# Performance work log

Measured on AMD Instinct MI355X. Metric: run time of the kernel, lower is better.

The kernel has to match this reference:

```python
import jax, jax.numpy as jnp
import numpy as np

H = 40  # HIDDEN_SIZE


def _gru_layer(x_tbi, Wih, Whh, bih, bhh):
    """PyTorch-convention GRU layer. x_tbi: (T, B, I). Returns (ys (T,B,H), h_T (B,H)).
    Gate order in stacked weights is (r, z, n) as in torch.nn.GRU:
      r = sigmoid(W_ir x + b_ir + W_hr h + b_hr)
      z = sigmoid(W_iz x + b_iz + W_hz h + b_hz)
      n = tanh(W_in x + b_in + r * (W_hn h + b_hn))
      h' = (1 - z) * n + z * h
    """
    # Precompute all input projections in one big GEMM: (T,B,3H)
    xg = jnp.einsum('tbi,gi->tbg', x_tbi, Wih) + bih
    B = x_tbi.shape[1]
    h0 = jnp.zeros((B, H), x_tbi.dtype)

    def step(h, xg_t):
        hg = h @ Whh.T + bhh                       # (B, 3H)
        xr, xz, xn = jnp.split(xg_t, 3, axis=-1)
        hr, hz, hn = jnp.split(hg, 3, axis=-1)
        r = jax.nn.sigmoid(xr + hr)
        z = jax.nn.sigmoid(xz + hz)
        n = jnp.tanh(xn + r * hn)
        h_new = (1.0 - z) * n + z * h
        return h_new, h_new

    hT, ys = jax.lax.scan(step, h0, xg)
    return ys, hT


def setup_inputs() -> dict:
    key = jax.random.key(0)
    ks = jax.random.split(key, 9)
    B, T, I = 4096, 256, 16
    s = 1.0 / np.sqrt(H)  # torch GRU init: U(-1/sqrt(H), 1/sqrt(H))
    u = lambda k, shape: jax.random.uniform(k, shape, jnp.float32, -s, s)
    return {
        "x": jax.random.normal(ks[0], (B, T, I), jnp.float32),
        "Wih0": u(ks[1], (3 * H, I)),
        "Whh0": u(ks[2], (3 * H, H)),
        "bih0": u(ks[3], (3 * H,)),
        "bhh0": u(ks[4], (3 * H,)),
        "Wih1": u(ks[5], (3 * H, H)),
        "Whh1": u(ks[6], (3 * H, H)),
        "bih1": u(ks[7], (3 * H,)),
        "bhh1": u(ks[8], (3 * H,)),
    }


def reference(x, Wih0, Whh0, bih0, bhh0, Wih1, Whh1, bih1, bhh1):
    # batch_first input (B,T,I) -> time-major (T,B,I) for scan
    x_tbi = jnp.transpose(x, (1, 0, 2))
    y0, _ = _gru_layer(x_tbi, Wih0, Whh0, bih0, bhh0)   # layer 0 full sequence
    _, hT = _gru_layer(y0, Wih1, Whh1, bih1, bhh1)      # layer 1 final state
    return hT  # (B, H) == h[-1]
```

## Files before the change

kernel.cpp:

```cpp
#include <hip/hip_runtime.h>

#define T_STEPS 256
#define HID 40
#define EPB 16
#define NTHR 1024
#define RR 56
#define PP (16 * RR)
#define OL1 (2 * PP)
#define STOT (4 * PP)

typedef __attribute__((ext_vector_type(8))) short bf16x8;
typedef __attribute__((ext_vector_type(4))) float f32x4;
typedef __attribute__((ext_vector_type(8))) float f32x8;
typedef __attribute__((ext_vector_type(4))) unsigned int u32x4;

__device__ __forceinline__ unsigned short bf16_rne(float v) {
    unsigned int x = __float_as_uint(v);
    unsigned int r = x + 0x7FFFu + ((x >> 16) & 1u);
    return (unsigned short)(r >> 16);
}
__device__ __forceinline__ unsigned short bf16_cvt(float v) {
    unsigned int r;
    asm("v_cvt_pk_bf16_f32 %0, %1, %2" : "=v"(r) : "v"(v), "v"(v));
    return (unsigned short)r;
}
__device__ __forceinline__ float sigm(float v) {
    return __builtin_amdgcn_rcpf(1.0f + __builtin_amdgcn_exp2f(-1.4426950408889634f * v));
}
__device__ __forceinline__ float tanh_f(float v) {
    return 1.0f - 2.0f * __builtin_amdgcn_rcpf(__builtin_amdgcn_exp2f(2.8853900817779268f * v) + 1.0f);
}

#define MF(A_, B_, C_) C_ = __builtin_amdgcn_mfma_f32_16x16x32_bf16(A_, B_, C_, 0, 0, 0)
#define PINV(v) asm volatile("" : "+v"(v))

#define BAR() do { \
    __builtin_amdgcn_sched_barrier(0); \
    asm volatile("s_waitcnt lgkmcnt(0)\n\ts_barrier" ::: "memory"); \
    __builtin_amdgcn_sched_barrier(0); \
} while (0)

__device__ bf16x8 afrag(const float* Whh, const float* Wih, int KX,
                        int rh, int rx, int c, int qrow) {
    bf16x8 f;
    #pragma unroll
    for (int j = 0; j < 8; ++j) f[j] = 0;
    #pragma unroll
    for (int j = 0; j < 8; ++j) {
        const int k = 32 * c + qrow * 8 + j;
        if (k < 40) {
            if (rh >= 0) f[j] = (short)bf16_rne(Whh[rh * 40 + k]);
        } else if (k < 40 + KX) {
            if (rx >= 0) f[j] = (short)bf16_rne(Wih[rx * KX + (k - 40)]);
        }
    }
    return f;
}

__global__ __launch_bounds__(NTHR, 4)
void gru2_kernel(const float* __restrict__ x,
                 const float* __restrict__ Wih0, const float* __restrict__ Whh0,
                 const float* __restrict__ bih0, const float* __restrict__ bhh0,
                 const float* __restrict__ Wih1, const float* __restrict__ Whh1,
                 const float* __restrict__ bih1, const float* __restrict__ bhh1,
                 float* __restrict__ out)
{
    __shared__ __align__(16) unsigned short S[STOT];

    const int tid  = threadIdx.x;
    const int wid  = tid >> 6;
    const int l    = tid & 63;
    const int col  = l & 15;
    const int qrow = l >> 4;
    const int ps   = (l & 15) & 3;
    const int pu   = (l & 15) >> 2;
    const int e0   = blockIdx.x * EPB;

    const bool isL1 = wid >= 6;
    const int  NT   = (!isL1 && wid < 4) ? 2 : 1;
    const int  TA   = isL1 ? (wid - 6) : (wid < 4 ? 2 * wid : wid + 4);
    const int  TB   = (NT == 2) ? TA + 1 : TA;
    const bool dB   = (NT != 2);

    const float* Whh = isL1 ? Whh1 : Whh0;
    const float* Wih = isL1 ? Wih1 : Wih0;
    const float* bih = isL1 ? bih1 : bih0;
    const float* bhh = isL1 ? bhh1 : bhh0;
    const int KX = isL1 ? 40 : 16;

    bf16x8 ZF;
    #pragma unroll
    for (int j = 0; j < 8; ++j) ZF[j] = 0;
    bf16x8 F00=ZF,F01=ZF,F02=ZF, F10=ZF,F11=ZF;
    f32x4 BB0, BB1;
    {
#define RRX(u, RH, RX) \
        const int RH = (ps == 2) ? -1 : (ps == 0 ? (u) : ps == 1 ? 40 + (u) : 80 + (u)); \
        const int RX = (ps == 3) ? -1 : (ps == 0 ? (u) : ps == 1 ? 40 + (u) : 80 + (u));
        {
            const int u0 = 4 * TA + pu;
            RRX(u0, rh0, rx0);
            F00 = afrag(Whh, Wih, KX, rh0, rx0, 0, qrow);
            F01 = afrag(Whh, Wih, KX, rh0, rx0, 1, qrow);
            if (isL1) F02 = afrag(Whh, Wih, KX, rh0, rx0, 2, qrow);
        }
        if (NT == 2) {
            const int u1 = 4 * TB + pu;
            RRX(u1, rh1, rx1);
            F10 = afrag(Whh, Wih, KX, rh1, rx1, 0, qrow);
            F11 = afrag(Whh, Wih, KX, rh1, rx1, 1, qrow);
        }
        const int uc0 = 4 * TA + qrow;
        const int uc1 = 4 * TB + qrow;
        BB0[0] = bih[uc0] + bhh[uc0];
        BB0[1] = bih[40 + uc0] + bhh[40 + uc0];
        BB0[2] = bih[80 + uc0];
        BB0[3] = bhh[80 + uc0];
        BB1[0] = dB ? 0.f : (bih[uc1] + bhh[uc1]);
        BB1[1] = dB ? 0.f : (bih[40 + uc1] + bhh[40 + uc1]);
        BB1[2] = dB ? 0.f : bih[80 + uc1];
        BB1[3] = dB ? 0.f : bhh[80 + uc1];
    }
    PINV(F00); PINV(F01); PINV(F02);
    PINV(F10); PINV(F11);
    PINV(BB0); PINV(BB1);

    const int rd0 = col * RR + 8 * qrow;
    const int rd1 = col * RR + 32;
    int g0, g1, g2;
    {
        auto ga = [&](int g) -> int {
            if (g < 5)  return OL1 + col * RR + 8 * g;
            if (g < 10) return col * RR + 8 * (g - 5);
            return col * RR;
        };
        g0 = ga(qrow);
        g1 = ga(4 + qrow);
        g2 = ga(8 + qrow);
    }
    const int w0  = col * RR + 4 * TA + qrow;
    const int w0b = col * RR + 4 * TB + qrow;
    const int w1  = OL1 + col * RR + 4 * TA + qrow;
    const bool usex = (qrow == 1) || (qrow == 2);
    unsigned short* Sb = &S[0];
    float hA0 = 0.f, hA1 = 0.f;

    for (int idx = tid; idx < STOT; idx += NTHR) Sb[idx] = 0;

    const float* xrow = x + (size_t)(e0 + col) * (T_STEPS * 16) + ((qrow == 2) ? 8 : 0);
    f32x8 XA, XB, XC, XD;
    #pragma unroll
    for (int j = 0; j < 8; ++j) { XA[j] = 0.f; XB[j] = 0.f; XC[j] = 0.f; XD[j] = 0.f; }
    if (!isL1) {
        XA = *(const f32x8*)(xrow);
        XB = *(const f32x8*)(xrow + 16);
        XC = *(const f32x8*)(xrow + 32);
        XD = *(const f32x8*)(xrow + 48);
    }
    __syncthreads();

#define GMATH(C, H) \
    const float r_ = sigm(C[0]); \
    const float z_ = sigm(C[1]); \
    const float n_ = tanh_f(C[2] + r_ * C[3]); \
    H = n_ + z_ * (H - n_);

#define BODY(RP, XQ) { \
    if (!isL1) { \
        if (t < T_STEPS) { \
            const bf16x8 S0 = *(const bf16x8*)(Sb + rd0 + (RP) * PP); \
            bf16x8 S1 = *(const bf16x8*)(Sb + rd1 + (RP) * PP); \
            unsigned int xw0, xw1, xw2, xw3; \
            asm("v_cvt_pk_bf16_f32 %0, %1, %2" : "=v"(xw0) : "v"(XQ[0]), "v"(XQ[1])); \
            asm("v_cvt_pk_bf16_f32 %0, %1, %2" : "=v"(xw1) : "v"(XQ[2]), "v"(XQ[3])); \
            asm("v_cvt_pk_bf16_f32 %0, %1, %2" : "=v"(xw2) : "v"(XQ[4]), "v"(XQ[5])); \
            asm("v_cvt_pk_bf16_f32 %0, %1, %2" : "=v"(xw3) : "v"(XQ[6]), "v"(XQ[7])); \
            if (t + 4 < T_STEPS) XQ = *(const f32x8*)(xrow + (t + 4) * 16); \
            u32x4 s1u = *(const u32x4*)&S1; \
            s1u[0] = usex ? xw0 : s1u[0]; \
            s1u[1] = usex ? xw1 : s1u[1]; \
            s1u[2] = usex ? xw2 : s1u[2]; \
            s1u[3] = usex ? xw3 : s1u[3]; \
            S1 = *(const bf16x8*)&s1u; \
            f32x4 c0 = __builtin_amdgcn_mfma_f32_16x16x32_bf16(F00, S0, BB0, 0, 0, 0); \
            MF(F01, S1, c0); \
            { GMATH(c0, hA0); Sb[w0 + (1 - (RP)) * PP] = bf16_cvt(hA0); } \
            if (NT == 2) { \
                f32x4 c1 = __builtin_amdgcn_mfma_f32_16x16x32_bf16(F10, S0, BB1, 0, 0, 0); \
                MF(F11, S1, c1); \
                GMATH(c1, hA1); Sb[w0b + (1 - (RP)) * PP] = bf16_cvt(hA1); \
            } \
        } \
    } else { \
        const bf16x8 S0 = *(const bf16x8*)(Sb + g0 + (RP) * PP); \
        const bf16x8 S1 = *(const bf16x8*)(Sb + g1 + (RP) * PP); \
        const bf16x8 S2 = *(const bf16x8*)(Sb + g2 + (RP) * PP); \
        f32x4 c = __builtin_amdgcn_mfma_f32_16x16x32_bf16(F00, S0, BB0, 0, 0, 0); \
        MF(F01, S1, c); MF(F02, S2, c); \
        if (t > 0) { GMATH(c, hA0); Sb[w1 + (1 - (RP)) * PP] = bf16_cvt(hA0); } \
    } \
    ++t; \
    BAR(); }

    int t = 0;
    #pragma unroll 1
    for (int it = 0; it < 64; ++it) {
        BODY(0, XA)
        BODY(1, XB)
        BODY(0, XC)
        BODY(1, XD)
    }
    BODY(0, XA)

    if (isL1) {
        out[(size_t)(e0 + col) * HID + 4 * TA + qrow] = hA0;
    }
}

extern "C" void kernel_launch(void* const* d_in, const int* in_sizes, int n_in,
                              void* d_out, int out_size, void* d_ws, size_t ws_size,
                              hipStream_t stream) {
    const float* x    = (const float*)d_in[0];
    const float* Wih0 = (const float*)d_in[1];
    const float* Whh0 = (const float*)d_in[2];
    const float* bih0 = (const float*)d_in[3];
    const float* bhh0 = (const float*)d_in[4];
    const float* Wih1 = (const float*)d_in[5];
    const float* Whh1 = (const float*)d_in[6];
    const float* bih1 = (const float*)d_in[7];
    const float* bhh1 = (const float*)d_in[8];
    float* out = (float*)d_out;

    dim3 grid(4096 / EPB), block(NTHR);
    hipLaunchKernelGGL(gru2_kernel, grid, block, 0, stream,
                       x, Wih0, Whh0, bih0, bhh0, Wih1, Whh1, bih1, bhh1, out);
}
```

Measured before the change: 234.9 us.

## Stage layer-0 input x through shared memory instead of per-wave register splicing

Layer-0 waves no longer each load 8 floats of x per lane, convert them to bf16 and splice them into the B fragment. Instead, 256 threads load one scalar each per step and write it into a widened shared row (RR0=72), which leaves room for x beside h. This removes redundant global loads and select operations from every layer-0 wave. The layer-0 and layer-1 buffers now use different strides. The sched_barrier fences around the barrier are also removed, giving the compiler more freedom to schedule, and shared memory grows somewhat.

```diff
diff --git a/kernel.cpp b/kernel.cpp
--- a/kernel.cpp
+++ b/kernel.cpp
@@ -4,15 +4,15 @@
 #define HID 40
 #define EPB 16
 #define NTHR 1024
-#define RR 56
-#define PP (16 * RR)
-#define OL1 (2 * PP)
-#define STOT (4 * PP)
+#define RR0 72
+#define RR1 56
+#define P0 (16 * RR0)
+#define P1 (16 * RR1)
+#define OL1 (2 * P0)
+#define STOT (2 * P0 + 2 * P1)
 
 typedef __attribute__((ext_vector_type(8))) short bf16x8;
 typedef __attribute__((ext_vector_type(4))) float f32x4;
-typedef __attribute__((ext_vector_type(8))) float f32x8;
-typedef __attribute__((ext_vector_type(4))) unsigned int u32x4;
 
 __device__ __forceinline__ unsigned short bf16_rne(float v) {
     unsigned int x = __float_as_uint(v);
@@ -34,11 +34,7 @@
 #define MF(A_, B_, C_) C_ = __builtin_amdgcn_mfma_f32_16x16x32_bf16(A_, B_, C_, 0, 0, 0)
 #define PINV(v) asm volatile("" : "+v"(v))
 
-#define BAR() do { \
-    __builtin_amdgcn_sched_barrier(0); \
-    asm volatile("s_waitcnt lgkmcnt(0)\n\ts_barrier" ::: "memory"); \
-    __builtin_amdgcn_sched_barrier(0); \
-} while (0)
+#define BAR() asm volatile("s_waitcnt lgkmcnt(0)\n\ts_barrier" ::: "memory")
 
 __device__ bf16x8 afrag(const float* Whh, const float* Wih, int KX,
                         int rh, int rx, int c, int qrow) {
@@ -125,37 +121,39 @@
     PINV(F10); PINV(F11);
     PINV(BB0); PINV(BB1);
 
-    const int rd0 = col * RR + 8 * qrow;
-    const int rd1 = col * RR + 32;
-    int g0, g1, g2;
+    const int rd0 = col * RR0 + 8 * qrow;
+    const int rd1 = rd0 + 32;
+    int g0p0, g0p1, g1p0, g1p1, g2p0, g2p1;
     {
-        auto ga = [&](int g) -> int {
-            if (g < 5)  return OL1 + col * RR + 8 * g;
-            if (g < 10) return col * RR + 8 * (g - 5);
-            return col * RR;
+        auto ga = [&](int g, int p) -> int {
+            if (g < 5)  return OL1 + p * P1 + col * RR1 + 8 * g;
+            if (g < 10) return p * P0 + col * RR0 + 8 * (g - 5);
+            return p * P0 + col * RR0;
         };
-        g0 = ga(qrow);
-        g1 = ga(4 + qrow);
-        g2 = ga(8 + qrow);
-    }
-    const int w0  = col * RR + 4 * TA + qrow;
-    const int w0b = col * RR + 4 * TB + qrow;
-    const int w1  = OL1 + col * RR + 4 * TA + qrow;
-    const bool usex = (qrow == 1) || (qrow == 2);
+        g0p0 = ga(qrow, 0);     g0p1 = ga(qrow, 1);
+        g1p0 = ga(4 + qrow, 0); g1p1 = ga(4 + qrow, 1);
+        g2p0 = ga(8 + qrow, 0); g2p1 = ga(8 + qrow, 1);
+    }
+    const int w0  = col * RR0 + 4 * TA + qrow;
+    const int w0b = col * RR0 + 4 * TB + qrow;
+    const int w1  = OL1 + col * RR1 + 4 * TA + qrow;
     unsigned short* Sb = &S[0];
     float hA0 = 0.f, hA1 = 0.f;
 
+    const bool xth = tid < 256;
+    const int xe = tid >> 4, xk = tid & 15;
+    const int xsl = xe * RR0 + 40 + xk;
+    const float* xrow = x + (size_t)(e0 + xe) * (T_STEPS * 16) + xk;
+
     for (int idx = tid; idx < STOT; idx += NTHR) Sb[idx] = 0;
-
-    const float* xrow = x + (size_t)(e0 + col) * (T_STEPS * 16) + ((qrow == 2) ? 8 : 0);
-    f32x8 XA, XB, XC, XD;
-    #pragma unroll
-    for (int j = 0; j < 8; ++j) { XA[j] = 0.f; XB[j] = 0.f; XC[j] = 0.f; XD[j] = 0.f; }
-    if (!isL1) {
-        XA = *(const f32x8*)(xrow);
-        XB = *(const f32x8*)(xrow + 16);
-        XC = *(const f32x8*)(xrow + 32);
-        XD = *(const f32x8*)(xrow + 48);
+    __syncthreads();
+    float XA = 0.f, XB = 0.f, XC = 0.f, XD = 0.f;
+    if (xth) {
+        Sb[xsl] = bf16_cvt(xrow[0]);
+        XA = xrow[16];
+        XB = xrow[32];
+        XC = xrow[48];
+        XD = xrow[64];
     }
     __syncthreads();
 
@@ -167,37 +165,29 @@
 
 #define BODY(RP, XQ) { \
     if (!isL1) { \
+        if (xth && t < T_STEPS - 1) { \
+            Sb[xsl + (1 - (RP)) * P0] = bf16_cvt(XQ); \
+            if (t + 5 < T_STEPS) XQ = xrow[(t + 5) * 16]; \
+        } \
         if (t < T_STEPS) { \
-            const bf16x8 S0 = *(const bf16x8*)(Sb + rd0 + (RP) * PP); \
-            bf16x8 S1 = *(const bf16x8*)(Sb + rd1 + (RP) * PP); \
-            unsigned int xw0, xw1, xw2, xw3; \
-            asm("v_cvt_pk_bf16_f32 %0, %1, %2" : "=v"(xw0) : "v"(XQ[0]), "v"(XQ[1])); \
-            asm("v_cvt_pk_bf16_f32 %0, %1, %2" : "=v"(xw1) : "v"(XQ[2]), "v"(XQ[3])); \
-            asm("v_cvt_pk_bf16_f32 %0, %1, %2" : "=v"(xw2) : "v"(XQ[4]), "v"(XQ[5])); \
-            asm("v_cvt_pk_bf16_f32 %0, %1, %2" : "=v"(xw3) : "v"(XQ[6]), "v"(XQ[7])); \
-            if (t + 4 < T_STEPS) XQ = *(const f32x8*)(xrow + (t + 4) * 16); \
-            u32x4 s1u = *(const u32x4*)&S1; \
-            s1u[0] = usex ? xw0 : s1u[0]; \
-            s1u[1] = usex ? xw1 : s1u[1]; \
-            s1u[2] = usex ? xw2 : s1u[2]; \
-            s1u[3] = usex ? xw3 : s1u[3]; \
-            S1 = *(const bf16x8*)&s1u; \
+            const bf16x8 S0 = *(const bf16x8*)(Sb + rd0 + (RP) * P0); \
+            const bf16x8 S1 = *(const bf16x8*)(Sb + rd1 + (RP) * P0); \
             f32x4 c0 = __builtin_amdgcn_mfma_f32_16x16x32_bf16(F00, S0, BB0, 0, 0, 0); \
             MF(F01, S1, c0); \
-            { GMATH(c0, hA0); Sb[w0 + (1 - (RP)) * PP] = bf16_cvt(hA0); } \
+            { GMATH(c0, hA0); Sb[w0 + (1 - (RP)) * P0] = bf16_cvt(hA0); } \
             if (NT == 2) { \
                 f32x4 c1 = __builtin_amdgcn_mfma_f32_16x16x32_bf16(F10, S0, BB1, 0, 0, 0); \
                 MF(F11, S1, c1); \
-                GMATH(c1, hA1); Sb[w0b + (1 - (RP)) * PP] = bf16_cvt(hA1); \
+                GMATH(c1, hA1); Sb[w0b + (1 - (RP)) * P0] = bf16_cvt(hA1); \
             } \
         } \
     } else { \
-        const bf16x8 S0 = *(const bf16x8*)(Sb + g0 + (RP) * PP); \
-        const bf16x8 S1 = *(const bf16x8*)(Sb + g1 + (RP) * PP); \
-        const bf16x8 S2 = *(const bf16x8*)(Sb + g2 + (RP) * PP); \
+        const bf16x8 S0 = *(const bf16x8*)(Sb + ((RP) ? g0p1 : g0p0)); \
+        const bf16x8 S1 = *(const bf16x8*)(Sb + ((RP) ? g1p1 : g1p0)); \
+        const bf16x8 S2 = *(const bf16x8*)(Sb + ((RP) ? g2p1 : g2p0)); \
         f32x4 c = __builtin_amdgcn_mfma_f32_16x16x32_bf16(F00, S0, BB0, 0, 0, 0); \
         MF(F01, S1, c); MF(F02, S2, c); \
-        if (t > 0) { GMATH(c, hA0); Sb[w1 + (1 - (RP)) * PP] = bf16_cvt(hA0); } \
+        if (t > 0) { GMATH(c, hA0); Sb[w1 + (1 - (RP)) * P1] = bf16_cvt(hA0); } \
     } \
     ++t; \
     BAR(); }
```

Result: faster. 202.0 us (-14.0%).
